# Kernel optimization log

Hardware: AMD Instinct MI355X
Metric: run time of the kernel (lower is better)

The kernel has to match this reference:

```python
import jax, jax.numpy as jnp
import numpy as np

COST_POINT = 0.1
COST_CLASS = 1.0
TOP_K = 4


def setup_inputs() -> dict:
    key = jax.random.key(0)
    k1, k2, k3, k4, k5 = jax.random.split(key, 5)
    bs, nq, ng, nc = 8, 16384, 1024, 5
    pred_coords = jax.random.uniform(k1, (bs, nq, 2), dtype=jnp.float32)
    pred_logits = jax.random.normal(k2, (bs, nq, nc), dtype=jnp.float32)
    gt_coords = jax.random.uniform(k3, (bs, ng, 2), dtype=jnp.float32)
    gt_labels = jax.random.randint(k4, (bs, ng), 0, nc, dtype=jnp.int64)
    gt_masks = jax.random.randint(k5, (bs, ng), 0, 2).astype(bool)
    return {
        "pred_coords": pred_coords,
        "pred_logits": pred_logits,
        "gt_coords": gt_coords,
        "gt_labels": gt_labels,
        "gt_masks": gt_masks,
    }


def reference(pred_coords, pred_logits, gt_coords, gt_labels, gt_masks):
    # pred_probs: [bs, nq, nc]
    pred_probs = jax.nn.softmax(pred_logits, axis=-1)
    # Euclidean cdist via ||a||^2 + ||b||^2 - 2ab, clamped for numerical safety.
    a2 = jnp.sum(pred_coords * pred_coords, axis=-1)  # [bs, nq]
    b2 = jnp.sum(gt_coords * gt_coords, axis=-1)      # [bs, ng]
    ab = jnp.einsum("bqd,bgd->bqg", pred_coords, gt_coords)
    cost_point = jnp.sqrt(jnp.maximum(a2[:, :, None] + b2[:, None, :] - 2.0 * ab, 0.0))  # [bs, nq, ng]
    # Gather class prob of each gt label for every query: [bs, nq, ng]
    cost_class = -jnp.take_along_axis(pred_probs, gt_labels[:, None, :], axis=2)
    C = COST_POINT * cost_point + COST_CLASS * cost_class
    C = jnp.where(gt_masks[:, None, :], C, jnp.inf)  # masked_fill(~mask, inf)
    # smallest-k along the query dim (-2): negate, move queries to last axis
    neg = -jnp.swapaxes(C, 1, 2)  # [bs, ng, nq]
    _, topk_idx = jax.lax.top_k(neg, TOP_K)  # [bs, ng, k]
    return jnp.swapaxes(topk_idx, 1, 2)  # [bs, k, ng]
```

## Files before the change

### kernel.cpp

```cpp
#include <hip/hip_runtime.h>
#include <cstdint>
#include <cstddef>

#define BS 8
#define NQ 16384
#define NG 1024
#define NC 5
#define BPB 32
#define LCAP 12032
#define CAP 400
#define PREF 0.55f
#define SLACK 0.1514214f
#define B2EPS 1e-3f

using u64 = unsigned long long;
typedef unsigned int u32;

__device__ __forceinline__ void ce(u64 &x, u64 &y) {
    u64 lo = x < y ? x : y;
    u64 hi = x < y ? y : x;
    x = lo; y = hi;
}
__device__ __forceinline__ void merge4(u64 a[4], u64 b0, u64 b1, u64 b2, u64 b3) {
    u64 m0 = a[0] < b3 ? a[0] : b3;
    u64 m1 = a[1] < b2 ? a[1] : b2;
    u64 m2 = a[2] < b1 ? a[2] : b1;
    u64 m3 = a[3] < b0 ? a[3] : b0;
    ce(m0, m2); ce(m1, m3); ce(m0, m1); ce(m2, m3);
    a[0] = m0; a[1] = m1; a[2] = m2; a[3] = m3;
}
__device__ __forceinline__ void kinsert(u64 kk[4], float cost, unsigned q) {
    unsigned uu = __float_as_uint(cost);
    uu ^= ((unsigned)((int)uu >> 31)) | 0x80000000u;
    u64 k = ((u64)uu << 32) | q;
    if (k < kk[3]) { kk[3] = k; ce(kk[2], kk[3]); ce(kk[1], kk[2]); ce(kk[0], kk[1]); }
}

__device__ __forceinline__ u32 umaxu(u32 a, u32 b) { return a > b ? a : b; }
__device__ __forceinline__ u32 uminu(u32 a, u32 b) { return a < b ? a : b; }
__device__ __forceinline__ void uce_desc(u32 &x, u32 &y) {
    u32 hi = umaxu(x, y), lo = uminu(x, y); x = hi; y = lo;
}
__device__ __forceinline__ void uinsert_desc(u32 k[4], u32 v) {
    u32 t;
    t = umaxu(k[0], v); v = uminu(k[0], v); k[0] = t;
    t = umaxu(k[1], v); v = uminu(k[1], v); k[1] = t;
    t = umaxu(k[2], v); v = uminu(k[2], v); k[2] = t;
    k[3] = umaxu(k[3], v);
}
__device__ __forceinline__ void umerge4_desc(u32 a[4], u32 b0, u32 b1, u32 b2, u32 b3) {
    u32 m0 = umaxu(a[0], b3), m1 = umaxu(a[1], b2), m2 = umaxu(a[2], b1), m3 = umaxu(a[3], b0);
    uce_desc(m0, m2); uce_desc(m1, m3); uce_desc(m0, m1); uce_desc(m2, m3);
    a[0] = m0; a[1] = m1; a[2] = m2; a[3] = m3;
}

#define SOFTMAX5(lg, X0, X1, X2, X3, X4, S)                                     \
    float X0 = (lg)[0], X1 = (lg)[1], X2 = (lg)[2], X3 = (lg)[3], X4 = (lg)[4]; \
    {                                                                           \
        float mx_ = fmaxf(fmaxf(fmaxf(X0, X1), fmaxf(X2, X3)), X4);             \
        X0 = expf(X0 - mx_); X1 = expf(X1 - mx_); X2 = expf(X2 - mx_);          \
        X3 = expf(X3 - mx_); X4 = expf(X4 - mx_);                               \
    }                                                                           \
    float S = X0 + X1 + X2 + X3 + X4;

__global__ __launch_bounds__(1024, 1) void fused_kernel(
        const float* __restrict__ pred_coords,
        const float* __restrict__ logits,
        const float* __restrict__ gt_coords,
        const int*   __restrict__ gt_labels,
        const int*   __restrict__ gt_masks,
        int*         __restrict__ out)
{
    const int tid = threadIdx.x;
    const int wv = tid >> 6, lane = tid & 63;
    const int b = blockIdx.x / BPB, part = blockIdx.x % BPB;

    __shared__ u64  lists[NC][CAP];
    __shared__ u32  L[LCAP];
    __shared__ u32  a2buf[15][4];
    __shared__ u32  a2cnt[15];
    __shared__ float Tsh[NC];
    __shared__ u32  lcount[NC];
    __shared__ u32  lcnt;
    __shared__ u32  flags;

    if (tid == 0) { lcnt = 0u; flags = 0u; }
    if (tid < NC) lcount[tid] = 0u;
    __syncthreads();

    const float* lgb = logits + (size_t)b * NQ * NC;

    #pragma unroll 2
    for (int r = 0; r < 16; ++r) {
        int q = r * 1024 + tid;
        const float* lg = lgb + (size_t)q * NC;
        float l0 = lg[0], l1 = lg[1], l2 = lg[2], l3 = lg[3], l4 = lg[4];
        float m = fmaxf(fmaxf(fmaxf(l0, l1), fmaxf(l2, l3)), l4);
        float e0 = __expf(l0 - m), e1 = __expf(l1 - m), e2 = __expf(l2 - m);
        float e3 = __expf(l3 - m), e4 = __expf(l4 - m);
        float s = ((e0 + e1) + (e2 + e3)) + e4;
        float ps = __builtin_amdgcn_rcpf(s);
        int cs = (l4 == m) ? 4 : (l3 == m) ? 3 : (l2 == m) ? 2 : (l1 == m) ? 1 : 0;

        bool pass = (ps >= PREF);
        u64 mk = __ballot(pass);
        if (mk) {
            u32 base = 0;
            if (lane == 0) base = atomicAdd(&lcnt, (u32)__popcll(mk));
            base = __shfl((int)base, 0, 64);
            if (pass) {
                u32 fb = __float_as_uint(ps);
                fb = fb > 0x3F7FFFFFu ? 0x3F7FFFFFu : fb;
                u32 key = (((fb >> 8) & 0x7FFFu) << 17) | ((u32)cs << 14) | (u32)q;
                u32 slot = base + (u32)__popcll(mk & ((1ull << lane) - 1ull));
                if (slot < LCAP) L[slot] = key;
            }
        }
    }
    __syncthreads();

    const u32 n = lcnt < LCAP ? lcnt : LCAP;
    if (tid == 0 && lcnt > LCAP) atomicOr(&flags, 0x1Fu);

    if (wv < 15) {
        int c = wv % 5, sl = wv / 5;
        u32 t4[4] = {0u, 0u, 0u, 0u};
        u32 cnt = 0u;
        for (u32 j = (u32)(sl * 64 + lane); j < n; j += 192u) {
            u32 k = L[j];
            if (((k >> 14) & 7u) == (u32)c) { uinsert_desc(t4, k); ++cnt; }
        }
        #pragma unroll
        for (int d = 1; d < 64; d <<= 1) {
            u32 b0 = (u32)__shfl_xor((int)t4[0], d, 64);
            u32 b1 = (u32)__shfl_xor((int)t4[1], d, 64);
            u32 b2 = (u32)__shfl_xor((int)t4[2], d, 64);
            u32 b3 = (u32)__shfl_xor((int)t4[3], d, 64);
            umerge4_desc(t4, b0, b1, b2, b3);
            cnt += (u32)__shfl_xor((int)cnt, d, 64);
        }
        if (lane == 0) {
            a2buf[wv][0] = t4[0]; a2buf[wv][1] = t4[1];
            a2buf[wv][2] = t4[2]; a2buf[wv][3] = t4[3];
            a2cnt[wv] = cnt;
        }
    }
    __syncthreads();

    if (tid < NC) {
        u32 t4[4] = {a2buf[tid][0], a2buf[tid][1], a2buf[tid][2], a2buf[tid][3]};
        umerge4_desc(t4, a2buf[tid + 5][0], a2buf[tid + 5][1], a2buf[tid + 5][2], a2buf[tid + 5][3]);
        umerge4_desc(t4, a2buf[tid + 10][0], a2buf[tid + 10][1], a2buf[tid + 10][2], a2buf[tid + 10][3]);
        u32 cnt = a2cnt[tid] + a2cnt[tid + 5] + a2cnt[tid + 10];
        float p4 = __uint_as_float(0x3F000000u | ((t4[3] >> 17) << 8));
        float T = p4 - SLACK;
        Tsh[tid] = T;
        if (cnt < 4u || T < PREF) atomicOr(&flags, 1u << tid);
    }
    __syncthreads();

    {
        u32 fl = flags;
        for (u32 j = (u32)tid; j < n; j += 1024u) {
            u32 k = L[j];
            u32 c = (k >> 14) & 7u;
            if ((fl >> c) & 1u) continue;
            float pf = __uint_as_float(0x3F000000u | ((k >> 17) << 8));
            if (pf >= Tsh[c] - B2EPS) {
                u32 q = k & 0x3FFFu;
                const float* lg = lgb + (size_t)q * NC;
                SOFTMAX5(lg, x0, x1, x2, x3, x4, s);
                float num = (c == 0) ? x0 : (c == 1) ? x1 : (c == 2) ? x2 : (c == 3) ? x3 : x4;
                float pe = num / s;
                u32 slot = atomicAdd(&lcount[c], 1u);
                if (slot < CAP) lists[c][slot] = ((u64)__float_as_uint(pe) << 32) | q;
            }
        }
    }
    __syncthreads();
    if (tid < NC && lcount[tid] > CAP) atomicOr(&flags, 1u << tid);
    __syncthreads();

    const float2* pc = reinterpret_cast<const float2*>(pred_coords) + (size_t)b * NQ;
    const u32 fl2 = flags;
    #pragma unroll 1
    for (int i = 0; i < 2; ++i) {
        int g = part * (NG / BPB) + i * 16 + wv;
        int m = gt_masks[b * NG + g];
        u64 kk[4] = {~0ull, ~0ull, ~0ull, ~0ull};
        if (m) {
            int c = gt_labels[b * NG + g];
            float2 gc = reinterpret_cast<const float2*>(gt_coords)[(size_t)b * NG + g];
            float gx = gc.x, gy = gc.y, gb2 = gc.x * gc.x + gc.y * gc.y;
            if (!((fl2 >> c) & 1u)) {
                u32 nn = lcount[c];
                for (u32 j = (u32)lane; j < nn; j += 64u) {
                    u64 e = lists[c][j];
                    float p = __uint_as_float((unsigned)(e >> 32));
                    unsigned qq = (unsigned)(e & 0xFFFFFFFFu);
                    float2 cq = pc[qq];
                    float d2 = fmaxf(cq.x * cq.x + cq.y * cq.y + gb2
                                     - 2.0f * (cq.x * gx + cq.y * gy), 0.0f);
                    kinsert(kk, 0.1f * sqrtf(d2) - p, qq);
                }
            } else {
                for (int q2 = lane; q2 < NQ; q2 += 64) {
                    const float* lg2 = lgb + (size_t)q2 * NC;
                    SOFTMAX5(lg2, y0, y1, y2, y3, y4, s2);
                    float num = (c == 0) ? y0 : (c == 1) ? y1 : (c == 2) ? y2 : (c == 3) ? y3 : y4;
                    float p = num / s2;
                    float2 cq = pc[q2];
                    float d2 = fmaxf(cq.x * cq.x + cq.y * cq.y + gb2
                                     - 2.0f * (cq.x * gx + cq.y * gy), 0.0f);
                    kinsert(kk, 0.1f * sqrtf(d2) - p, (unsigned)q2);
                }
            }
            #pragma unroll
            for (int d = 1; d < 64; d <<= 1) {
                u64 b0 = __shfl_xor(kk[0], d, 64);
                u64 b1 = __shfl_xor(kk[1], d, 64);
                u64 b2_ = __shfl_xor(kk[2], d, 64);
                u64 b3 = __shfl_xor(kk[3], d, 64);
                merge4(kk, b0, b1, b2_, b3);
            }
        }
        if (lane < 4) {
            u64 sel = (lane == 0) ? kk[0] : (lane == 1) ? kk[1] : (lane == 2) ? kk[2] : kk[3];
            int idx = m ? (int)(sel & 0xFFFFFFFFull) : lane;
            out[((size_t)(b * 4 + lane) << 10) + g] = idx;
        }
    }
}

extern "C" void kernel_launch(void* const* d_in, const int* in_sizes, int n_in,
                              void* d_out, int out_size, void* d_ws, size_t ws_size,
                              hipStream_t stream) {
    const float* pred_coords = (const float*)d_in[0];
    const float* pred_logits = (const float*)d_in[1];
    const float* gt_coords   = (const float*)d_in[2];
    const int*   gt_labels   = (const int*)d_in[3];
    const int*   gt_masks    = (const int*)d_in[4];
    int* out = (int*)d_out;

    fused_kernel<<<BS * BPB, 1024, 0, stream>>>(
        pred_coords, pred_logits, gt_coords, gt_labels, gt_masks, out);
}
```

Baseline: 28.56 us.

## Use per-wave candidate lists and float4 logit loads in prefilter phase

```diff
diff --git a/kernel.cpp b/kernel.cpp
--- a/kernel.cpp
+++ b/kernel.cpp
@@ -7,8 +7,8 @@
 #define NG 1024
 #define NC 5
 #define BPB 32
-#define LCAP 12032
-#define CAP 400
+#define WCAP 704
+#define CAP 448
 #define PREF 0.55f
 #define SLACK 0.1514214f
 #define B2EPS 1e-3f
@@ -62,6 +62,16 @@
         X3 = expf(X3 - mx_); X4 = expf(X4 - mx_);                               \
     }                                                                           \
     float S = X0 + X1 + X2 + X3 + X4;
+
+#define PSTAR(L0, L1, L2, L3, L4, PS, CS)                                       \
+    float PS; int CS;                                                           \
+    {                                                                           \
+        float m_ = fmaxf(fmaxf(fmaxf(L0, L1), fmaxf(L2, L3)), L4);              \
+        float e0_ = __expf(L0 - m_), e1_ = __expf(L1 - m_), e2_ = __expf(L2 - m_); \
+        float e3_ = __expf(L3 - m_), e4_ = __expf(L4 - m_);                     \
+        PS = __builtin_amdgcn_rcpf(((e0_ + e1_) + (e2_ + e3_)) + e4_);          \
+        CS = (L4 == m_) ? 4 : (L3 == m_) ? 3 : (L2 == m_) ? 2 : (L1 == m_) ? 1 : 0; \
+    }
 
 __global__ __launch_bounds__(1024, 1) void fused_kernel(
         const float* __restrict__ pred_coords,
@@ -74,95 +84,110 @@
     const int tid = threadIdx.x;
     const int wv = tid >> 6, lane = tid & 63;
     const int b = blockIdx.x / BPB, part = blockIdx.x % BPB;
+    const u64 lmlt = (1ull << lane) - 1ull;
 
     __shared__ u64  lists[NC][CAP];
-    __shared__ u32  L[LCAP];
-    __shared__ u32  a2buf[15][4];
-    __shared__ u32  a2cnt[15];
+    __shared__ u32  L[16][WCAP];
+    __shared__ u32  a2buf[16][NC][4];
+    __shared__ u32  a2cnt[16][NC];
     __shared__ float Tsh[NC];
     __shared__ u32  lcount[NC];
-    __shared__ u32  lcnt;
     __shared__ u32  flags;
 
-    if (tid == 0) { lcnt = 0u; flags = 0u; }
+    if (tid == 0) flags = 0u;
     if (tid < NC) lcount[tid] = 0u;
     __syncthreads();
 
     const float* lgb = logits + (size_t)b * NQ * NC;
+    u32* Lw = L[wv];
+    u32 mycnt = 0u;
 
     #pragma unroll 2
-    for (int r = 0; r < 16; ++r) {
-        int q = r * 1024 + tid;
-        const float* lg = lgb + (size_t)q * NC;
-        float l0 = lg[0], l1 = lg[1], l2 = lg[2], l3 = lg[3], l4 = lg[4];
-        float m = fmaxf(fmaxf(fmaxf(l0, l1), fmaxf(l2, l3)), l4);
-        float e0 = __expf(l0 - m), e1 = __expf(l1 - m), e2 = __expf(l2 - m);
-        float e3 = __expf(l3 - m), e4 = __expf(l4 - m);
-        float s = ((e0 + e1) + (e2 + e3)) + e4;
-        float ps = __builtin_amdgcn_rcpf(s);
-        int cs = (l4 == m) ? 4 : (l3 == m) ? 3 : (l2 == m) ? 2 : (l1 == m) ? 1 : 0;
-
-        bool pass = (ps >= PREF);
-        u64 mk = __ballot(pass);
-        if (mk) {
-            u32 base = 0;
-            if (lane == 0) base = atomicAdd(&lcnt, (u32)__popcll(mk));
-            base = __shfl((int)base, 0, 64);
-            if (pass) {
-                u32 fb = __float_as_uint(ps);
-                fb = fb > 0x3F7FFFFFu ? 0x3F7FFFFFu : fb;
-                u32 key = (((fb >> 8) & 0x7FFFu) << 17) | ((u32)cs << 14) | (u32)q;
-                u32 slot = base + (u32)__popcll(mk & ((1ull << lane) - 1ull));
-                if (slot < LCAP) L[slot] = key;
-            }
-        }
-    }
-    __syncthreads();
-
-    const u32 n = lcnt < LCAP ? lcnt : LCAP;
-    if (tid == 0 && lcnt > LCAP) atomicOr(&flags, 0x1Fu);
-
-    if (wv < 15) {
-        int c = wv % 5, sl = wv / 5;
-        u32 t4[4] = {0u, 0u, 0u, 0u};
-        u32 cnt = 0u;
-        for (u32 j = (u32)(sl * 64 + lane); j < n; j += 192u) {
-            u32 k = L[j];
-            if (((k >> 14) & 7u) == (u32)c) { uinsert_desc(t4, k); ++cnt; }
+    for (int r = 0; r < 4; ++r) {
+        int qb = r * 4096 + tid * 4;
+        const float4* pv = reinterpret_cast<const float4*>(lgb + (size_t)qb * NC);
+        float4 v0 = pv[0], v1 = pv[1], v2 = pv[2], v3 = pv[3], v4 = pv[4];
+        PSTAR(v0.x, v0.y, v0.z, v0.w, v1.x, psA, csA);
+        PSTAR(v1.y, v1.z, v1.w, v2.x, v2.y, psB, csB);
+        PSTAR(v2.z, v2.w, v3.x, v3.y, v3.z, psC, csC);
+        PSTAR(v3.w, v4.x, v4.y, v4.z, v4.w, psD, csD);
+        #define APP(PS, CS, QQ)                                                     \
+        {                                                                           \
+            bool pass = ((PS) >= PREF);                                             \
+            u64 mk = __ballot(pass);                                                \
+            if (mk) {                                                               \
+                if (pass) {                                                         \
+                    u32 fb = __float_as_uint(PS);                                   \
+                    fb = fb > 0x3F7FFFFFu ? 0x3F7FFFFFu : fb;                       \
+                    u32 key = (((fb >> 8) & 0x7FFFu) << 17) | ((u32)(CS) << 14) | (u32)(QQ); \
+                    u32 slot = mycnt + (u32)__popcll(mk & lmlt);                    \
+                    if (slot < WCAP) Lw[slot] = key;                                \
+                }                                                                   \
+                mycnt += (u32)__popcll(mk);                                         \
+            }                                                                       \
+        }
+        APP(psA, csA, qb + 0)
+        APP(psB, csB, qb + 1)
+        APP(psC, csC, qb + 2)
+        APP(psD, csD, qb + 3)
+        #undef APP
+    }
+    if (lane == 0 && mycnt > WCAP) atomicOr(&flags, 0x1Fu);
+    const u32 nW = mycnt < WCAP ? mycnt : WCAP;
+
+    {
+        u32 t40[4] = {0u,0u,0u,0u}, t41[4] = {0u,0u,0u,0u}, t42[4] = {0u,0u,0u,0u};
+        u32 t43[4] = {0u,0u,0u,0u}, t44[4] = {0u,0u,0u,0u};
+        u32 c0 = 0u, c1 = 0u, c2 = 0u, c3 = 0u, c4 = 0u;
+        for (u32 j = (u32)lane; j < nW; j += 64u) {
+            u32 k = Lw[j];
+            u32 c = (k >> 14) & 7u;
+            uinsert_desc(t40, c == 0u ? k : 0u); c0 += (c == 0u);
+            uinsert_desc(t41, c == 1u ? k : 0u); c1 += (c == 1u);
+            uinsert_desc(t42, c == 2u ? k : 0u); c2 += (c == 2u);
+            uinsert_desc(t43, c == 3u ? k : 0u); c3 += (c == 3u);
+            uinsert_desc(t44, c == 4u ? k : 0u); c4 += (c == 4u);
         }
         #pragma unroll
         for (int d = 1; d < 64; d <<= 1) {
-            u32 b0 = (u32)__shfl_xor((int)t4[0], d, 64);
-            u32 b1 = (u32)__shfl_xor((int)t4[1], d, 64);
-            u32 b2 = (u32)__shfl_xor((int)t4[2], d, 64);
-            u32 b3 = (u32)__shfl_xor((int)t4[3], d, 64);
-            umerge4_desc(t4, b0, b1, b2, b3);
-            cnt += (u32)__shfl_xor((int)cnt, d, 64);
+            #define RED(T, C)                                                       \
+                umerge4_desc(T, (u32)__shfl_xor((int)T[0], d, 64),                  \
+                                (u32)__shfl_xor((int)T[1], d, 64),                  \
+                                (u32)__shfl_xor((int)T[2], d, 64),                  \
+                                (u32)__shfl_xor((int)T[3], d, 64));                 \
+                C += (u32)__shfl_xor((int)C, d, 64);
+            RED(t40, c0) RED(t41, c1) RED(t42, c2) RED(t43, c3) RED(t44, c4)
+            #undef RED
         }
         if (lane == 0) {
-            a2buf[wv][0] = t4[0]; a2buf[wv][1] = t4[1];
-            a2buf[wv][2] = t4[2]; a2buf[wv][3] = t4[3];
-            a2cnt[wv] = cnt;
+            #define ST(I, T, C)                                                     \
+                a2buf[wv][I][0] = T[0]; a2buf[wv][I][1] = T[1];                     \
+                a2buf[wv][I][2] = T[2]; a2buf[wv][I][3] = T[3]; a2cnt[wv][I] = C;
+            ST(0, t40, c0) ST(1, t41, c1) ST(2, t42, c2) ST(3, t43, c3) ST(4, t44, c4)
+            #undef ST
         }
     }
     __syncthreads();
 
     if (tid < NC) {
-        u32 t4[4] = {a2buf[tid][0], a2buf[tid][1], a2buf[tid][2], a2buf[tid][3]};
-        umerge4_desc(t4, a2buf[tid + 5][0], a2buf[tid + 5][1], a2buf[tid + 5][2], a2buf[tid + 5][3]);
-        umerge4_desc(t4, a2buf[tid + 10][0], a2buf[tid + 10][1], a2buf[tid + 10][2], a2buf[tid + 10][3]);
-        u32 cnt = a2cnt[tid] + a2cnt[tid + 5] + a2cnt[tid + 10];
+        u32 t4[4] = {a2buf[0][tid][0], a2buf[0][tid][1], a2buf[0][tid][2], a2buf[0][tid][3]};
+        u32 cnt = a2cnt[0][tid];
+        #pragma unroll
+        for (int w = 1; w < 16; ++w) {
+            umerge4_desc(t4, a2buf[w][tid][0], a2buf[w][tid][1], a2buf[w][tid][2], a2buf[w][tid][3]);
+            cnt += a2cnt[w][tid];
+        }
         float p4 = __uint_as_float(0x3F000000u | ((t4[3] >> 17) << 8));
         float T = p4 - SLACK;
         Tsh[tid] = T;
-        if (cnt < 4u || T < PREF) atomicOr(&flags, 1u << tid);
+        if (cnt < 4u || T < PREF + 1e-5f) atomicOr(&flags, 1u << tid);
     }
     __syncthreads();
 
     {
         u32 fl = flags;
-        for (u32 j = (u32)tid; j < n; j += 1024u) {
-            u32 k = L[j];
+        for (u32 j = (u32)lane; j < nW; j += 64u) {
+            u32 k = Lw[j];
             u32 c = (k >> 14) & 7u;
             if ((fl >> c) & 1u) continue;
             float pf = __uint_as_float(0x3F000000u | ((k >> 17) << 8));
@@ -193,7 +218,7 @@
             float2 gc = reinterpret_cast<const float2*>(gt_coords)[(size_t)b * NG + g];
             float gx = gc.x, gy = gc.y, gb2 = gc.x * gc.x + gc.y * gc.y;
             if (!((fl2 >> c) & 1u)) {
-                u32 nn = lcount[c];
+                u32 nn = lcount[c] < CAP ? lcount[c] : CAP;
                 for (u32 j = (u32)lane; j < nn; j += 64u) {
                     u64 e = lists[c][j];
                     float p = __uint_as_float((unsigned)(e >> 32));
```

New measurement: 29.77 us. +4.3%, slower.
